# Kernel optimization log

Hardware: AMD Instinct MI355X
Metric: run time of the kernel (lower is better)

## Reference

```python
import jax, jax.numpy as jnp
import numpy as np

MEAN, STD = 0.1307, 0.3081  # standard MNIST Normalization layer
FC = [784, 2048, 2048, 2048, 2048, 10]


def _forward_boxes(W, b, low, high):
    # swap bounds where weights are negative (interval arithmetic)
    Wn = jnp.where(W < 0, W, 0.0)
    Wp = jnp.where(W >= 0, W, 0.0)
    low_out = high @ Wn.T + low @ Wp.T + b
    high_out = low @ Wn.T + high @ Wp.T + b
    return low_out, high_out


def _abstract_relu(x, low, high):
    # vectorized DeepPoly relaxation (original loops per neuron)
    crossing = (low < 0) & (high > 0)
    denom = jnp.where(crossing, high - low, 1.0)  # safe denom
    ub_slope = jnp.where(crossing, high / denom, 0.0)
    ub_int = jnp.where(crossing, -(low * high) / denom, 0.0)
    lam = jnp.where(low * low > high * high, 0.0, 1.0)  # minimum-area lambda
    keep = jnp.where(high <= 0.0, 0.0, 1.0)  # identity diag unless dead neuron
    w_high = jnp.where(crossing, ub_slope, keep)
    w_low = jnp.where(crossing, lam, keep)
    b_high = ub_int
    x_out = jnp.maximum(x, 0.0)
    return x_out, w_low * low, w_high * high + b_high, (w_low, w_high, b_high)


def _back_sub_relu(M, w_high, w_low, b_high, is_high):
    # vectorized version of the original double python loop; w_* are the
    # relu diagonals ([in]), M is the accumulated backsub matrix [out,in]
    mask = (w_high != 0.0).astype(M.dtype)
    if is_high:
        out = jnp.where(M > 0, M * w_high, M * w_low) * mask
        bias = (jnp.maximum(M, 0.0) * mask) @ b_high
    else:
        out = jnp.where(M > 0, M * w_low, M * w_high) * mask
        bias = (jnp.minimum(M, 0.0) * mask) @ b_high
    return out, bias


def _back_sub(records, low0, high0, out_size):
    dt = low0.dtype
    Wl = jnp.eye(out_size, dtype=dt)
    Wh = jnp.eye(out_size, dtype=dt)
    bl = jnp.zeros(out_size, dtype=dt)
    bh = jnp.zeros(out_size, dtype=dt)
    for kind, data in reversed(records):
        if kind == 'linear':
            W, b = data
            bh = bh + Wh @ b
            bl = bl + Wl @ b
            Wh = Wh @ W
            Wl = Wl @ W
        else:  # relu
            wl, wh, bhr = data
            Wh, dbh = _back_sub_relu(Wh, wh, wl, bhr, True)
            Wl, dbl = _back_sub_relu(Wl, wh, wl, bhr, False)
            bh = bh + dbh
            bl = bl + dbl
    low_out, _ = _forward_boxes(Wl, bl, low0, high0)
    _, high_out = _forward_boxes(Wh, bh, low0, high0)
    return low_out, high_out


def _forward(x, low, high, params):
    norm = lambda t: ((t - MEAN) / STD).reshape(-1)
    x, low, high = norm(x), norm(low), norm(high)
    low0, high0 = low, high
    records = []
    n = len(params)
    for i, (W, b) in enumerate(params):
        x = W @ x + b
        records.append(('linear', (W, b)))
        # box bounds from forward_boxes are immediately replaced by backsub
        low, high = _back_sub(records, low0, high0, W.shape[0])
        if i + 1 < n:
            x, low, high, rdata = _abstract_relu(x, low, high)
            records.append(('relu', rdata))
    return x, low, high


def setup_inputs() -> dict:
    key = jax.random.key(0)
    ks = jax.random.split(key, 11)
    x = jax.random.normal(ks[0], (1, 1, 28, 28), dtype=jnp.float32)
    eps = 0.05
    inp = {"x": x, "low": x - eps, "high": x + eps}
    for i in range(5):
        fi, fo = FC[i], FC[i + 1]
        inp[f"W{i+1}"] = jax.random.normal(ks[1 + 2 * i], (fo, fi), dtype=jnp.float32) * float(1.0 / np.sqrt(fi))
        inp[f"b{i+1}"] = jax.random.normal(ks[2 + 2 * i], (fo,), dtype=jnp.float32) * 0.01
    return inp


def reference(x, low, high, W1, b1, W2, b2, W3, b3, W4, b4, W5, b5):
    params = [(W1, b1), (W2, b2), (W3, b3), (W4, b4), (W5, b5)]
    return _forward(x, low, high, params)
```

## Files before the change

### kernel.cpp

```cpp
#include <hip/hip_runtime.h>
#include <hip/hip_bf16.h>


#define MEAN_C 0.1307f
#define STD_C  0.3081f

#define OFF_X0     0u
#define OFF_X1     2048u
#define OFF_L0     4096u
#define OFF_H0     5120u
#define OFF_WL     6144u
#define OFF_WH     14336u
#define OFF_BHR    22528u
#define OFF_BOXA   30720u
#define OFF_BOXB   34816u
#define OFF_BIASA  38912u
#define OFF_BIASB  43008u
#define OFF_B20    47104u
#define OFF_W0TH   47136u
#define OFF_W0TL   964640u
#define OFF_W1TH   1882144u
#define OFF_W1TL   3979296u
#define OFF_W2TH   6076448u
#define OFF_W2TL   8173600u
#define OFF_AH0    10270752u
#define OFF_AL0    14465056u
#define OFF_AH1    18659360u
#define OFF_AL1    22853664u
#define OFF_PPA    18659360u
#define OFF_PPB    18987040u
#define OFF_PPC    19314720u
#define OFF_PPD    19642400u

typedef _Float16 half8 __attribute__((ext_vector_type(8)));
typedef float floatx4 __attribute__((ext_vector_type(4)));

__device__ __forceinline__ void gl2lds16(const void* g, void* l) {
    __builtin_amdgcn_global_load_lds(
        (const __attribute__((address_space(1))) unsigned int*)g,
        (__attribute__((address_space(3))) unsigned int*)l, 16, 0, 0);
}

__device__ __forceinline__ float blockReduce256(float v) {
    #pragma unroll
    for (int o = 32; o > 0; o >>= 1) v += __shfl_down(v, o, 64);
    __shared__ float sred[4];
    int w = threadIdx.x >> 6;
    if ((threadIdx.x & 63) == 0) sred[w] = v;
    __syncthreads();
    float r = 0.f;
    if (threadIdx.x == 0) r = sred[0] + sred[1] + sred[2] + sred[3];
    return r;
}

__device__ __forceinline__ float2 blockReduce256x2(float a, float b) {
    #pragma unroll
    for (int o = 32; o > 0; o >>= 1) {
        a += __shfl_down(a, o, 64);
        b += __shfl_down(b, o, 64);
    }
    __shared__ float sa[4], sb[4];
    int w = threadIdx.x >> 6;
    if ((threadIdx.x & 63) == 0) { sa[w] = a; sb[w] = b; }
    __syncthreads();
    float2 r = {0.f, 0.f};
    if (threadIdx.x == 0) {
        r.x = sa[0] + sa[1] + sa[2] + sa[3];
        r.y = sb[0] + sb[1] + sb[2] + sb[3];
    }
    return r;
}

__device__ __forceinline__ void relu_rec_calc(float h, float l,
                                              float& vwl, float& vwh, float& vbh) {
    if (h <= 0.f)      { vwl = 0.f; vwh = 0.f; vbh = 0.f; }
    else if (l >= 0.f) { vwl = 1.f; vwh = 1.f; vbh = 0.f; }
    else {
        float d = h - l;
        vwh = h / d;
        vbh = -(l * h) / d;
        vwl = (l * l > h * h) ? 0.f : 1.f;
    }
}

__global__ void k_norm(const float* __restrict__ x, const float* __restrict__ lo,
                       const float* __restrict__ hi, float* __restrict__ ws) {
    int i = blockIdx.x * blockDim.x + threadIdx.x;
    if (i < 784) {
        ws[OFF_X0 + i] = (x[i]  - MEAN_C) / STD_C;
        ws[OFF_L0 + i] = (lo[i] - MEAN_C) / STD_C;
        ws[OFF_H0 + i] = (hi[i] - MEAN_C) / STD_C;
    } else if (i < 896) {
        ws[OFF_L0 + i] = 0.f;
        ws[OFF_H0 + i] = 0.f;
    }
}

__global__ void k_fboxes0(const float* __restrict__ W0, const float* __restrict__ b0,
                          const float* __restrict__ x0,
                          const float* __restrict__ lo0, const float* __restrict__ hi0,
                          float* __restrict__ box, float* __restrict__ xout) {
    int r = blockIdx.x;
    int srow = r & 2047;
    int is_high = r < 2048;
    const float* Wr = W0 + (size_t)srow * 784;
    float acc = 0.f, accx = 0.f;
    for (int c = threadIdx.x; c < 784; c += 256) {
        float m = Wr[c];
        if (is_high) acc += (m < 0.f) ? m * lo0[c] : m * hi0[c];
        else         acc += (m < 0.f) ? m * hi0[c] : m * lo0[c];
        accx += m * x0[c];
    }
    float2 rr = blockReduce256x2(acc, accx);
    if (threadIdx.x == 0) {
        box[r] = rr.x + b0[srow];
        if (is_high) xout[r] = rr.y + b0[r];
    }
}

__global__ __launch_bounds__(256) void k_relu_split(
        const float* __restrict__ Wi, const float* __restrict__ xin,
        const float* __restrict__ boxPrev, const float* __restrict__ biasPrev,
        float* __restrict__ recWL, float* __restrict__ recWH, float* __restrict__ recBH,
        const float* __restrict__ bj, const float* __restrict__ bvi,
        float* __restrict__ bias, float* __restrict__ boxOut,
        float* __restrict__ xout,
        _Float16* __restrict__ Ahi, _Float16* __restrict__ Alo) {
    int row = blockIdx.x;
    int is_high = row < 2048;
    int srow = row & 2047;
    const float* src = Wi + (size_t)srow * 2048;
    int c0 = threadIdx.x * 8;
    float mv[8], bxh[8], bxl[8], abj[8], ax[8];
    *(float4*)&mv[0]  = *(const float4*)(src + c0);
    *(float4*)&mv[4]  = *(const float4*)(src + c0 + 4);
    *(float4*)&bxh[0] = *(const float4*)(boxPrev + c0);
    *(float4*)&bxh[4] = *(const float4*)(boxPrev + c0 + 4);
    *(float4*)&bxl[0] = *(const float4*)(boxPrev + 2048 + c0);
    *(float4*)&bxl[4] = *(const float4*)(boxPrev + 2048 + c0 + 4);
    *(float4*)&abj[0] = *(const float4*)(bj + c0);
    *(float4*)&abj[4] = *(const float4*)(bj + c0 + 4);
    *(float4*)&ax[0]  = *(const float4*)(xin + c0);
    *(float4*)&ax[4]  = *(const float4*)(xin + c0 + 4);
    if (biasPrev) {
        float ph[8], pl[8];
        *(float4*)&ph[0] = *(const float4*)(biasPrev + c0);
        *(float4*)&ph[4] = *(const float4*)(biasPrev + c0 + 4);
        *(float4*)&pl[0] = *(const float4*)(biasPrev + 2048 + c0);
        *(float4*)&pl[4] = *(const float4*)(biasPrev + 2048 + c0 + 4);
        #pragma unroll
        for (int e = 0; e < 8; e++) { bxh[e] += ph[e]; bxl[e] += pl[e]; }
    }
    float acc = 0.f, accx = 0.f;
    float rl[8], rh[8], rb[8];
    half8 hi, lo;
    #pragma unroll
    for (int e = 0; e < 8; e++) {
        relu_rec_calc(bxh[e], bxl[e], rl[e], rh[e], rb[e]);
        float m = mv[e];
        float t, bt;
        if (is_high) { t = (m > 0.f) ? m * rh[e] : m * rl[e]; bt = fmaxf(m, 0.f) * rb[e]; }
        else         { t = (m > 0.f) ? m * rl[e] : m * rh[e]; bt = fminf(m, 0.f) * rb[e]; }
        acc += bt + t * abj[e];
        accx += m * fmaxf(ax[e], 0.f);
        _Float16 h = (_Float16)t;
        hi[e] = h;
        lo[e] = (_Float16)(t - (float)h);
    }
    *(half8*)(Ahi + (size_t)row * 2048 + c0) = hi;
    *(half8*)(Alo + (size_t)row * 2048 + c0) = lo;
    if (row == 0) {
        *(float4*)(recWL + c0) = *(float4*)&rl[0];
        *(float4*)(recWL + c0 + 4) = *(float4*)&rl[4];
        *(float4*)(recWH + c0) = *(float4*)&rh[0];
        *(float4*)(recWH + c0 + 4) = *(float4*)&rh[4];
        *(float4*)(recBH + c0) = *(float4*)&rb[0];
        *(float4*)(recBH + c0 + 4) = *(float4*)&rb[4];
    }
    float2 rr = blockReduce256x2(acc, accx);
    if (threadIdx.x == 0) {
        bias[row] = bvi[srow] + rr.x;
        boxOut[row] = 0.f;
        if (is_high) xout[row] = rr.y + bvi[row];
    }
}

__global__ void k_transpose_split(const float* __restrict__ W, int NC,
                                  _Float16* __restrict__ Thi,
                                  _Float16* __restrict__ Tlo) {
    __shared__ float s[32][33];
    int c = threadIdx.x & 31;
    int r = threadIdx.x >> 5;
    #pragma unroll
    for (int rr = 0; rr < 4; rr++) {
        int k = blockIdx.y * 32 + r + rr * 8;
        int n = blockIdx.x * 32 + c;
        float v = (n < NC) ? W[(size_t)k * NC + n] : 0.f;
        s[c][r + rr * 8] = v;
    }
    __syncthreads();
    #pragma unroll
    for (int rr = 0; rr < 4; rr++) {
        int nl = r + rr * 8;
        float v = s[nl][c];
        _Float16 h = (_Float16)v;
        size_t o = (size_t)(blockIdx.x * 32 + nl) * 2048 + blockIdx.y * 32 + c;
        Thi[o] = h;
        Tlo[o] = (_Float16)(v - (float)h);
    }
}

template<int NT, int EPI>
__global__ __launch_bounds__(256, 2) void k_gemm(
        const _Float16* __restrict__ Ah, const _Float16* __restrict__ Al,
        const _Float16* __restrict__ Bh, const _Float16* __restrict__ Bl,
        const float* __restrict__ wl, const float* __restrict__ wh,
        const float* __restrict__ bhr, const float* __restrict__ bj,
        float* __restrict__ bias,
        _Float16* __restrict__ oAh, _Float16* __restrict__ oAl,
        const float* __restrict__ lo0, const float* __restrict__ hi0,
        float* __restrict__ box) {
    __shared__ _Float16 sAh[2][128 * 32], sAl[2][128 * 32];
    __shared__ _Float16 sBh[2][NT * 32 * 32], sBl[2][NT * 32 * 32];
    int tid = threadIdx.x;
    int row0 = blockIdx.y * 128, col0 = blockIdx.x * (NT * 32);

    int cr = tid >> 2;
    int q  = (tid & 3) ^ ((cr >> 1) & 3);
    const _Float16* gAh0 = Ah + (size_t)(row0 + cr) * 2048 + q * 8;
    const _Float16* gAh1 = gAh0 + (size_t)64 * 2048;
    const _Float16* gAl0 = Al + (size_t)(row0 + cr) * 2048 + q * 8;
    const _Float16* gAl1 = gAl0 + (size_t)64 * 2048;
    const _Float16* gBh0 = Bh + (size_t)(col0 + cr) * 2048 + q * 8;
    const _Float16* gBl0 = Bl + (size_t)(col0 + cr) * 2048 + q * 8;
    const _Float16* gBh1 = gBh0 + (size_t)64 * 2048;
    const _Float16* gBl1 = gBl0 + (size_t)64 * 2048;
    int loff = tid * 8;

    int lane = tid & 63, wv = tid >> 6;
    int wm = wv & 1, wn = wv >> 1;
    int l15 = lane & 15, lq = lane >> 4;
    int soff = (lq ^ ((l15 >> 1) & 3)) * 8;
    int arow = wm * 64 + l15;
    int brow = wn * (NT * 16) + l15;

    floatx4 acc[4][NT];
    floatx4 z = {0.f, 0.f, 0.f, 0.f};
    #pragma unroll
    for (int i = 0; i < 4; i++)
        #pragma unroll
        for (int j = 0; j < NT; j++) acc[i][j] = z;

    auto STAGE = [&](int b, int k0) {
        gl2lds16(gAh0 + k0, &sAh[b][loff]);
        gl2lds16(gAh1 + k0, &sAh[b][loff + 2048]);
        gl2lds16(gAl0 + k0, &sAl[b][loff]);
        gl2lds16(gAl1 + k0, &sAl[b][loff + 2048]);
        gl2lds16(gBh0 + k0, &sBh[b][loff]);
        gl2lds16(gBl0 + k0, &sBl[b][loff]);
        if (NT == 4) {
            gl2lds16(gBh1 + k0, &sBh[b][loff + 2048]);
            gl2lds16(gBl1 + k0, &sBl[b][loff + 2048]);
        }
    };

    STAGE(0, 0);
    STAGE(1, 32);
    if constexpr (NT == 4) asm volatile("s_waitcnt vmcnt(8)" ::: "memory");
    else                   asm volatile("s_waitcnt vmcnt(6)" ::: "memory");
    __builtin_amdgcn_s_barrier();
    __builtin_amdgcn_sched_barrier(0);

    for (int t = 0; t < 64; ++t) {
        int cur = t & 1;
        half8 bh[NT], bl[NT], ah4[4], al4[4];
        #pragma unroll
        for (int nt = 0; nt < NT; nt++) {
            bh[nt] = *(const half8*)&sBh[cur][(brow + nt * 16) * 32 + soff];
            bl[nt] = *(const half8*)&sBl[cur][(brow + nt * 16) * 32 + soff];
        }
        #pragma unroll
        for (int mt = 0; mt < 4; mt++) {
            ah4[mt] = *(const half8*)&sAh[cur][(arow + mt * 16) * 32 + soff];
            al4[mt] = *(const half8*)&sAl[cur][(arow + mt * 16) * 32 + soff];
        }
        asm volatile("s_waitcnt lgkmcnt(0)" ::: "memory");
        __builtin_amdgcn_sched_barrier(0);
        __builtin_amdgcn_s_barrier();
        __builtin_amdgcn_sched_barrier(0);
        if (t < 62) STAGE(cur, (t + 2) * 32);
        #pragma unroll
        for (int mt = 0; mt < 4; mt++) {
            #pragma unroll
            for (int nt = 0; nt < NT; nt++) {
                acc[mt][nt] = __builtin_amdgcn_mfma_f32_16x16x32_f16(ah4[mt], bh[nt], acc[mt][nt], 0, 0, 0);
                acc[mt][nt] = __builtin_amdgcn_mfma_f32_16x16x32_f16(al4[mt], bh[nt], acc[mt][nt], 0, 0, 0);
                acc[mt][nt] = __builtin_amdgcn_mfma_f32_16x16x32_f16(ah4[mt], bl[nt], acc[mt][nt], 0, 0, 0);
            }
        }
        if (t < 63) {
            if (t < 62) {
                if constexpr (NT == 4) asm volatile("s_waitcnt vmcnt(8)" ::: "memory");
                else                   asm volatile("s_waitcnt vmcnt(6)" ::: "memory");
            } else {
                asm volatile("s_waitcnt vmcnt(0)" ::: "memory");
            }
            __builtin_amdgcn_s_barrier();
            __builtin_amdgcn_sched_barrier(0);
        }
    }

    int is_high = row0 < 2048;
    float bsum[4][4];
    #pragma unroll
    for (int mt = 0; mt < 4; mt++)
        #pragma unroll
        for (int r = 0; r < 4; r++) bsum[mt][r] = 0.f;

    #pragma unroll
    for (int nt = 0; nt < NT; nt++) {
        int gc = col0 + wn * (NT * 16) + nt * 16 + l15;
        if (EPI == 0) {
            float cwl = wl[gc], cwh = wh[gc], cbh = bhr[gc], cbj = bj[gc];
            #pragma unroll
            for (int mt = 0; mt < 4; mt++) {
                #pragma unroll
                for (int r = 0; r < 4; r++) {
                    float m = acc[mt][nt][r];
                    float t, bt;
                    if (is_high) { t = (m > 0.f) ? m * cwh : m * cwl; bt = fmaxf(m, 0.f) * cbh; }
                    else         { t = (m > 0.f) ? m * cwl : m * cwh; bt = fminf(m, 0.f) * cbh; }
                    bsum[mt][r] += bt + t * cbj;
                    int grow = row0 + wm * 64 + mt * 16 + lq * 4 + r;
                    size_t o = (size_t)grow * 2048 + gc;
                    _Float16 h = (_Float16)t;
                    oAh[o] = h;
                    oAl[o] = (_Float16)(t - (float)h);
                }
            }
        } else {
            float clo = lo0[gc], chi = hi0[gc];
            #pragma unroll
            for (int mt = 0; mt < 4; mt++) {
                #pragma unroll
                for (int r = 0; r < 4; r++) {
                    float m = acc[mt][nt][r];
                    float contrib;
                    if (is_high) contrib = (m < 0.f) ? m * clo : m * chi;
                    else         contrib = (m < 0.f) ? m * chi : m * clo;
                    bsum[mt][r] += contrib;
                }
            }
        }
    }
    #pragma unroll
    for (int mt = 0; mt < 4; mt++) {
        #pragma unroll
        for (int r = 0; r < 4; r++) {
            float v = bsum[mt][r];
            v += __shfl_xor(v, 1);
            v += __shfl_xor(v, 2);
            v += __shfl_xor(v, 4);
            v += __shfl_xor(v, 8);
            if (l15 == 0) {
                int grow = row0 + wm * 64 + mt * 16 + lq * 4 + r;
                if (EPI == 0) atomicAdd(&bias[grow], v);
                else          atomicAdd(&box[grow], v);
            }
        }
    }
}

__global__ void k_relu_rec(const float* __restrict__ box, const float* __restrict__ bias,
                           float* __restrict__ wl, float* __restrict__ wh,
                           float* __restrict__ bhr) {
    int i = blockIdx.x * blockDim.x + threadIdx.x;
    float h = box[i] + bias[i];
    float l = box[2048 + i] + bias[2048 + i];
    float vwl, vwh, vbh;
    relu_rec_calc(h, l, vwl, vwh, vbh);
    wl[i] = vwl; wh[i] = vwh; bhr[i] = vbh;
}

__global__ __launch_bounds__(256) void k_skinny2(
        const float* __restrict__ src, int bcast,
        const float* __restrict__ wl, const float* __restrict__ wh,
        const float* __restrict__ W, int N, float* __restrict__ Ppart) {
    __shared__ float sA[20 * 256];
    __shared__ float sRed[20 * 128];
    int ky = blockIdx.y, k0 = ky * 256;
    int tid = threadIdx.x;
    for (int idx = tid; idx < 20 * 256; idx += 256) {
        int r = idx >> 8, c = idx & 255;
        int gc = k0 + c;
        float m;
        if (bcast) m = src[(size_t)(r % 10) * 2048 + gc];
        else {
            m = 0.f;
            #pragma unroll
            for (int p = 0; p < 8; p++)
                m += src[(size_t)p * 40960 + (size_t)r * 2048 + gc];
        }
        float t = (r < 10) ? ((m > 0.f) ? m * wh[gc] : m * wl[gc])
                           : ((m > 0.f) ? m * wl[gc] : m * wh[gc]);
        sA[idx] = t;
    }
    __syncthreads();
    int c = blockIdx.x * 128 + (tid & 127);
    int kh = tid >> 7;
    float acc[20];
    #pragma unroll
    for (int r = 0; r < 20; r++) acc[r] = 0.f;
    if (c < N) {
        const float* Wp = W + (size_t)(k0 + kh * 128) * N + c;
        for (int kk = 0; kk < 128; kk++) {
            float w = Wp[(size_t)kk * N];
            #pragma unroll
            for (int r = 0; r < 20; r++) acc[r] += sA[r * 256 + kh * 128 + kk] * w;
        }
    }
    if (kh == 1 && c < N) {
        #pragma unroll
        for (int r = 0; r < 20; r++) sRed[r * 128 + (tid & 127)] = acc[r];
    }
    __syncthreads();
    if (kh == 0 && c < N) {
        #pragma unroll
        for (int r = 0; r < 20; r++)
            Ppart[(size_t)ky * 40960 + (size_t)r * 2048 + c] =
                acc[r] + sRed[r * 128 + (tid & 127)];
    }
}

__global__ void k_bias20(const float* __restrict__ W4,
                         const float* __restrict__ PPa, const float* __restrict__ PPb,
                         const float* __restrict__ PPc,
                         const float* __restrict__ WLr, const float* __restrict__ WHr,
                         const float* __restrict__ BHr,
                         const float* __restrict__ b0, const float* __restrict__ b1,
                         const float* __restrict__ b2, const float* __restrict__ b3,
                         const float* __restrict__ b4,
                         const float* __restrict__ x3,
                         float* __restrict__ bias20, float* __restrict__ out) {
    int row = blockIdx.x;
    int is_high = row < 10;
    int srow = row % 10;
    float acc = 0.f, accx = 0.f;
    for (int c = threadIdx.x; c < 2048; c += 256) {
        {
            float m = W4[(size_t)srow * 2048 + c];
            float wlv = WLr[3 * 2048 + c], whv = WHr[3 * 2048 + c], bhv = BHr[3 * 2048 + c];
            float t  = is_high ? ((m > 0.f) ? m * whv : m * wlv) : ((m > 0.f) ? m * wlv : m * whv);
            float bt = is_high ? fmaxf(m, 0.f) * bhv : fminf(m, 0.f) * bhv;
            acc += bt + t * b3[c];
            accx += m * fmaxf(x3[c], 0.f);
        }
        {
            float m = 0.f;
            #pragma unroll
            for (int p = 0; p < 8; p++) m += PPa[(size_t)p * 40960 + (size_t)row * 2048 + c];
            float wlv = WLr[2 * 2048 + c], whv = WHr[2 * 2048 + c], bhv = BHr[2 * 2048 + c];
            float t  = is_high ? ((m > 0.f) ? m * whv : m * wlv) : ((m > 0.f) ? m * wlv : m * whv);
            float bt = is_high ? fmaxf(m, 0.f) * bhv : fminf(m, 0.f) * bhv;
            acc += bt + t * b2[c];
        }
        {
            float m = 0.f;
            #pragma unroll
            for (int p = 0; p < 8; p++) m += PPb[(size_t)p * 40960 + (size_t)row * 2048 + c];
            float wlv = WLr[1 * 2048 + c], whv = WHr[1 * 2048 + c], bhv = BHr[1 * 2048 + c];
            float t  = is_high ? ((m > 0.f) ? m * whv : m * wlv) : ((m > 0.f) ? m * wlv : m * whv);
            float bt = is_high ? fmaxf(m, 0.f) * bhv : fminf(m, 0.f) * bhv;
            acc += bt + t * b1[c];
        }
        {
            float m = 0.f;
            #pragma unroll
            for (int p = 0; p < 8; p++) m += PPc[(size_t)p * 40960 + (size_t)row * 2048 + c];
            float wlv = WLr[c], whv = WHr[c], bhv = BHr[c];
            float t  = is_high ? ((m > 0.f) ? m * whv : m * wlv) : ((m > 0.f) ? m * wlv : m * whv);
            float bt = is_high ? fmaxf(m, 0.f) * bhv : fminf(m, 0.f) * bhv;
            acc += bt + t * b0[c];
        }
    }
    float2 rr = blockReduce256x2(acc, accx);
    if (threadIdx.x == 0) {
        bias20[row] = b4[srow] + rr.x;
        if (is_high) out[row] = b4[row] + rr.y;
    }
}

__global__ void k_fbox20(const float* __restrict__ Ppart,
                         const float* __restrict__ bias20,
                         const float* __restrict__ lo0, const float* __restrict__ hi0,
                         float* __restrict__ out) {
    int row = blockIdx.x;
    int is_high = row < 10;
    float acc = 0.f;
    for (int c = threadIdx.x; c < 784; c += 256) {
        float m = 0.f;
        #pragma unroll
        for (int p = 0; p < 8; p++)
            m += Ppart[(size_t)p * 40960 + (size_t)row * 2048 + c];
        if (is_high) acc += (m < 0.f) ? m * lo0[c] : m * hi0[c];
        else         acc += (m < 0.f) ? m * hi0[c] : m * lo0[c];
    }
    acc = blockReduce256(acc);
    if (threadIdx.x == 0) {
        float v = acc + bias20[row];
        out[is_high ? (20 + row) : row] = v;
    }
}

extern "C" void kernel_launch(void* const* d_in, const int* in_sizes, int n_in,
                              void* d_out, int out_size, void* d_ws, size_t ws_size,
                              hipStream_t stream) {
    const float* x_in  = (const float*)d_in[0];
    const float* lo_in = (const float*)d_in[1];
    const float* hi_in = (const float*)d_in[2];
    const float* W[5];
    const float* bv[5];
    for (int i = 0; i < 5; i++) {
        W[i]  = (const float*)d_in[3 + 2 * i];
        bv[i] = (const float*)d_in[4 + 2 * i];
    }
    float* ws = (float*)d_ws;
    float* out = (float*)d_out;

    float* X[2]    = {ws + OFF_X0, ws + OFF_X1};
    float* lo0     = ws + OFF_L0;
    float* hi0     = ws + OFF_H0;
    float* BOX[2]  = {ws + OFF_BOXA, ws + OFF_BOXB};
    float* BIAS[2] = {ws + OFF_BIASA, ws + OFF_BIASB};
    float* b20     = ws + OFF_B20;
    float* PPa     = ws + OFF_PPA;
    float* PPb     = ws + OFF_PPB;
    float* PPc     = ws + OFF_PPC;
    float* PPd     = ws + OFF_PPD;
    _Float16* WT_H[3] = {(_Float16*)(ws + OFF_W0TH), (_Float16*)(ws + OFF_W1TH),
                         (_Float16*)(ws + OFF_W2TH)};
    _Float16* WT_L[3] = {(_Float16*)(ws + OFF_W0TL), (_Float16*)(ws + OFF_W1TL),
                         (_Float16*)(ws + OFF_W2TL)};
    _Float16* AH[2] = {(_Float16*)(ws + OFF_AH0), (_Float16*)(ws + OFF_AH1)};
    _Float16* AL[2] = {(_Float16*)(ws + OFF_AL0), (_Float16*)(ws + OFF_AL1)};
    float* WLr = ws + OFF_WL;
    float* WHr = ws + OFF_WH;
    float* BHr = ws + OFF_BHR;

    k_norm<<<4, 256, 0, stream>>>(x_in, lo_in, hi_in, ws);
    k_transpose_split<<<dim3(28, 64), 256, 0, stream>>>(W[0], 784, WT_H[0], WT_L[0]);
    k_transpose_split<<<dim3(64, 64), 256, 0, stream>>>(W[1], 2048, WT_H[1], WT_L[1]);
    k_transpose_split<<<dim3(64, 64), 256, 0, stream>>>(W[2], 2048, WT_H[2], WT_L[2]);

    k_fboxes0<<<4096, 256, 0, stream>>>(W[0], bv[0], X[0], lo0, hi0, BOX[0], X[1]);

    int xcur = 1, bprev = 0;
    const float* biasPrev = nullptr;
    for (int i = 1; i <= 3; i++) {
        int xnxt = xcur ^ 1;
        int bcur = bprev ^ 1;
        float* biasCur = BIAS[(i - 1) & 1];
        k_relu_split<<<4096, 256, 0, stream>>>(
            W[i], X[xcur], BOX[bprev], biasPrev,
            WLr + (i - 1) * 2048, WHr + (i - 1) * 2048, BHr + (i - 1) * 2048,
            bv[i - 1], bv[i], biasCur, BOX[bcur], X[xnxt], AH[0], AL[0]);
        int p = 0;
        for (int j = i - 1; j >= 1; j--) {
            k_gemm<4, 0><<<dim3(16, 32), 256, 0, stream>>>(
                AH[p], AL[p], WT_H[j], WT_L[j],
                WLr + (j - 1) * 2048, WHr + (j - 1) * 2048,
                BHr + (j - 1) * 2048, bv[j - 1], biasCur,
                AH[p ^ 1], AL[p ^ 1], nullptr, nullptr, nullptr);
            p ^= 1;
        }
        k_gemm<2, 1><<<dim3(14, 32), 256, 0, stream>>>(
            AH[p], AL[p], WT_H[0], WT_L[0],
            nullptr, nullptr, nullptr, nullptr, nullptr,
            nullptr, nullptr, lo0, hi0, BOX[bcur]);
        biasPrev = biasCur;
        bprev = bcur;
        xcur = xnxt;
    }
    k_relu_rec<<<8, 256, 0, stream>>>(BOX[bprev], BIAS[0],
                                      WLr + 3 * 2048, WHr + 3 * 2048, BHr + 3 * 2048);

    k_skinny2<<<dim3(16, 8), 256, 0, stream>>>(W[4], 1,
        WLr + 3 * 2048, WHr + 3 * 2048, W[3], 2048, PPa);
    k_skinny2<<<dim3(16, 8), 256, 0, stream>>>(PPa, 0,
        WLr + 2 * 2048, WHr + 2 * 2048, W[2], 2048, PPb);
    k_skinny2<<<dim3(16, 8), 256, 0, stream>>>(PPb, 0,
        WLr + 1 * 2048, WHr + 1 * 2048, W[1], 2048, PPc);
    k_skinny2<<<dim3(7, 8), 256, 0, stream>>>(PPc, 0,
        WLr, WHr, W[0], 784, PPd);
    k_bias20<<<20, 256, 0, stream>>>(W[4], PPa, PPb, PPc,
        WLr, WHr, BHr, bv[0], bv[1], bv[2], bv[3], bv[4], X[xcur], b20, out);
    k_fbox20<<<20, 256, 0, stream>>>(PPd, b20, lo0, hi0, out);
}
```

Measured before the change: 869.4 us.

## Double-buffer register fragments so LDS reads overlap MFMA in GEMM mainloop

Restructures the GEMM main loop into a two-step unrolled pipeline with two sets of register fragments. The LDS reads for the next k-tile are issued before the MFMA cluster on the current fragments, and the global-to-LDS staging is issued alongside. The goal is to hide LDS read latency behind matrix work and drop one barrier per iteration. In exchange it doubles fragment register use, which may hurt occupancy under launch_bounds(256,2), and it now waits on vmcnt(0) every step instead of keeping one stage of global loads in flight.

```diff
diff --git a/kernel.cpp b/kernel.cpp
--- a/kernel.cpp
+++ b/kernel.cpp
@@ -224,6 +224,7 @@
     __shared__ _Float16 sBh[2][NT * 32 * 32], sBl[2][NT * 32 * 32];
     int tid = threadIdx.x;
     int row0 = blockIdx.y * 128, col0 = blockIdx.x * (NT * 32);
+    constexpr int LPT = (NT == 4) ? 8 : 6;
 
     int cr = tid >> 2;
     int q  = (tid & 3) ^ ((cr >> 1) & 3);
@@ -264,51 +265,67 @@
         }
     };
 
+    half8 b0h[NT], b0l[NT], a0h[4], a0l[4];
+    half8 b1h[NT], b1l[NT], a1h[4], a1l[4];
+
+#define READ_FRAGS(BH_, BL_, AH_, AL_, B_)                                   \
+    {   _Pragma("unroll")                                                    \
+        for (int nt = 0; nt < NT; nt++) {                                    \
+            BH_[nt] = *(const half8*)&sBh[B_][(brow + nt * 16) * 32 + soff]; \
+            BL_[nt] = *(const half8*)&sBl[B_][(brow + nt * 16) * 32 + soff]; \
+        }                                                                    \
+        _Pragma("unroll")                                                    \
+        for (int mt = 0; mt < 4; mt++) {                                     \
+            AH_[mt] = *(const half8*)&sAh[B_][(arow + mt * 16) * 32 + soff]; \
+            AL_[mt] = *(const half8*)&sAl[B_][(arow + mt * 16) * 32 + soff]; \
+        }                                                                    \
+    }
+
+#define MFMA_CLUSTER(BH_, BL_, AH_, AL_)                                     \
+    {   _Pragma("unroll")                                                    \
+        for (int mt = 0; mt < 4; mt++) {                                     \
+            _Pragma("unroll")                                                \
+            for (int nt = 0; nt < NT; nt++) {                                \
+                acc[mt][nt] = __builtin_amdgcn_mfma_f32_16x16x32_f16(AH_[mt], BH_[nt], acc[mt][nt], 0, 0, 0); \
+                acc[mt][nt] = __builtin_amdgcn_mfma_f32_16x16x32_f16(AL_[mt], BH_[nt], acc[mt][nt], 0, 0, 0); \
+                acc[mt][nt] = __builtin_amdgcn_mfma_f32_16x16x32_f16(AH_[mt], BL_[nt], acc[mt][nt], 0, 0, 0); \
+            }                                                                \
+        }                                                                    \
+    }
+
     STAGE(0, 0);
     STAGE(1, 32);
-    if constexpr (NT == 4) asm volatile("s_waitcnt vmcnt(8)" ::: "memory");
-    else                   asm volatile("s_waitcnt vmcnt(6)" ::: "memory");
+    asm volatile("s_waitcnt vmcnt(%0)" :: "n"(LPT) : "memory");
+    __builtin_amdgcn_s_barrier();
+    READ_FRAGS(b0h, b0l, a0h, a0l, 0);
+    asm volatile("s_waitcnt lgkmcnt(0) vmcnt(0)" ::: "memory");
     __builtin_amdgcn_s_barrier();
     __builtin_amdgcn_sched_barrier(0);
 
-    for (int t = 0; t < 64; ++t) {
-        int cur = t & 1;
-        half8 bh[NT], bl[NT], ah4[4], al4[4];
-        #pragma unroll
-        for (int nt = 0; nt < NT; nt++) {
-            bh[nt] = *(const half8*)&sBh[cur][(brow + nt * 16) * 32 + soff];
-            bl[nt] = *(const half8*)&sBl[cur][(brow + nt * 16) * 32 + soff];
-        }
-        #pragma unroll
-        for (int mt = 0; mt < 4; mt++) {
-            ah4[mt] = *(const half8*)&sAh[cur][(arow + mt * 16) * 32 + soff];
-            al4[mt] = *(const half8*)&sAl[cur][(arow + mt * 16) * 32 + soff];
-        }
-        asm volatile("s_waitcnt lgkmcnt(0)" ::: "memory");
+    for (int tt = 0; tt < 32; ++tt) {
+        int t0 = 2 * tt;
+        READ_FRAGS(b1h, b1l, a1h, a1l, 1);
+        if (t0 < 62) STAGE(0, (t0 + 2) * 32);
+        __builtin_amdgcn_sched_barrier(0);
+        MFMA_CLUSTER(b0h, b0l, a0h, a0l);
+        asm volatile("s_waitcnt lgkmcnt(0) vmcnt(0)" ::: "memory");
         __builtin_amdgcn_sched_barrier(0);
         __builtin_amdgcn_s_barrier();
         __builtin_amdgcn_sched_barrier(0);
-        if (t < 62) STAGE(cur, (t + 2) * 32);
-        #pragma unroll
-        for (int mt = 0; mt < 4; mt++) {
-            #pragma unroll
-            for (int nt = 0; nt < NT; nt++) {
-                acc[mt][nt] = __builtin_amdgcn_mfma_f32_16x16x32_f16(ah4[mt], bh[nt], acc[mt][nt], 0, 0, 0);
-                acc[mt][nt] = __builtin_amdgcn_mfma_f32_16x16x32_f16(al4[mt], bh[nt], acc[mt][nt], 0, 0, 0);
-                acc[mt][nt] = __builtin_amdgcn_mfma_f32_16x16x32_f16(ah4[mt], bl[nt], acc[mt][nt], 0, 0, 0);
-            }
-        }
-        if (t < 63) {
-            if (t < 62) {
-                if constexpr (NT == 4) asm volatile("s_waitcnt vmcnt(8)" ::: "memory");
-                else                   asm volatile("s_waitcnt vmcnt(6)" ::: "memory");
-            } else {
-                asm volatile("s_waitcnt vmcnt(0)" ::: "memory");
-            }
+        int t1 = t0 + 1;
+        if (t1 < 63) READ_FRAGS(b0h, b0l, a0h, a0l, 0);
+        if (t1 < 62) STAGE(1, (t1 + 2) * 32);
+        __builtin_amdgcn_sched_barrier(0);
+        MFMA_CLUSTER(b1h, b1l, a1h, a1l);
+        if (t1 < 63) {
+            asm volatile("s_waitcnt lgkmcnt(0) vmcnt(0)" ::: "memory");
+            __builtin_amdgcn_sched_barrier(0);
             __builtin_amdgcn_s_barrier();
             __builtin_amdgcn_sched_barrier(0);
         }
     }
+#undef READ_FRAGS
+#undef MFMA_CLUSTER
 
     int is_high = row0 < 2048;
     float bsum[4][4];
```

Result: no change. 872.7 us (+0.4%).
